# Optimization experiments

Hardware: AMD Instinct MI355X
Metric: run time of the kernel (lower is better)

The kernel has to match this reference:

```python
import jax, jax.numpy as jnp
import numpy as np

B, HW, NL = 32, 1024, 64
VD, LD, H = 1024, 768, 8
EPS = 1e-5


def _bn(x, g, b):
    # x: [B, L, C]; BatchNorm1d (train mode, batch stats) over (B, L) per channel
    m = x.mean(axis=(0, 1), keepdims=True)
    v = x.var(axis=(0, 1), keepdims=True)
    return (x - m) * jax.lax.rsqrt(v + EPS) * g + b


def _inorm(x):
    # x: [B, L, C]; InstanceNorm1d (no affine): normalize over L per (sample, channel)
    m = x.mean(axis=1, keepdims=True)
    v = x.var(axis=1, keepdims=True)
    return (x - m) * jax.lax.rsqrt(v + EPS)


def _sdpa(q_in, k_in, v_in, qw, qb, kw, kb, vw, vb, ow, ob, query_mask=None, key_mask=None):
    b, nq, d = q_in.shape
    nk = k_in.shape[1]
    dk = d // H
    q = (q_in @ qw.T + qb).reshape(b, nq, H, dk).transpose(0, 2, 1, 3)  # [b,h,nq,dk]
    k = (k_in @ kw.T + kb).reshape(b, nk, H, dk).transpose(0, 2, 1, 3)  # [b,h,nk,dk]
    v = (v_in @ vw.T + vb).reshape(b, nk, H, dk).transpose(0, 2, 1, 3)  # [b,h,nk,dk]
    if query_mask is not None:
        q = q * query_mask.reshape(b, 1, nq, 1)
    if key_mask is not None:
        k = k * key_mask.reshape(b, 1, nk, 1)
        v = v * key_mask.reshape(b, 1, nk, 1)
    att = jnp.einsum('bhqd,bhkd->bhqk', q, k) / (dk ** 0.5)
    att = jax.nn.softmax(att, axis=-1)
    out = jnp.einsum('bhqk,bhkd->bhqd', att, v)
    out = out.transpose(0, 2, 1, 3).reshape(b, nq, d)
    return out @ ow.T + ob, att


def setup_inputs() -> dict:
    key = jax.random.key(0)
    ks = iter(jax.random.split(key, 64))
    d = {
        'src': jax.random.normal(next(ks), (B, HW, VD), jnp.float32),
        'lan': jax.random.normal(next(ks), (B, NL, LD), jnp.float32),
        'pos_embed': jax.random.normal(next(ks), (B, HW, VD), jnp.float32),
        'lan_attmask': jnp.ones((B, NL), jnp.float32),
        'ip_w': jax.random.normal(next(ks), (VD, VD), jnp.float32) * 0.02,
        'ip_b': jnp.zeros((VD,), jnp.float32),
        'ip_g': jnp.ones((VD,), jnp.float32),
        'ip_beta': jnp.zeros((VD,), jnp.float32),
        'lp_w': jax.random.normal(next(ks), (VD, LD), jnp.float32) * 0.02,
        'lp_b': jnp.zeros((VD,), jnp.float32),
        'mem_tok': jax.random.normal(next(ks), (1, VD), jnp.float32) * 0.02,
        'neg_mem_tok': jax.random.normal(next(ks), (1, VD), jnp.float32) * 0.02,
    }
    for pre in ('vl', 'mf', 'ff'):
        for nm in ('q', 'k', 'v', 'o'):
            d[f'{pre}_{nm}w'] = jax.random.normal(next(ks), (VD, VD), jnp.float32) * 0.02
            d[f'{pre}_{nm}b'] = jnp.zeros((VD,), jnp.float32)
    d['op_w'] = jax.random.normal(next(ks), (VD, VD), jnp.float32) * 0.02
    d['op_b'] = jnp.zeros((VD,), jnp.float32)
    d['op_g'] = jnp.ones((VD,), jnp.float32)
    d['op_beta'] = jnp.zeros((VD,), jnp.float32)
    return d


def reference(src, lan, pos_embed, lan_attmask, ip_w, ip_b, ip_g, ip_beta, lp_w, lp_b,
              mem_tok, neg_mem_tok,
              vl_qw, vl_qb, vl_kw, vl_kb, vl_vw, vl_vb, vl_ow, vl_ob,
              mf_qw, mf_qb, mf_kw, mf_kb, mf_vw, mf_vb, mf_ow, mf_ob,
              ff_qw, ff_qb, ff_kw, ff_kb, ff_vw, ff_vb, ff_ow, ff_ob,
              op_w, op_b, op_g, op_beta):
    # input/lan projections (Conv1d k=1 == per-token linear), BN on vision path
    src_p = _bn(src @ ip_w.T + ip_b, ip_g, ip_beta)          # [B,HW,VD]
    lan_p = lan @ lp_w.T + lp_b                              # [B,NL,VD]

    # stage 1: vision-language fuse (query = language, multiplicative query mask)
    vl_out, vl_att = _sdpa(lan_p, src_p, src_p,
                           vl_qw, vl_qb, vl_kw, vl_kb, vl_vw, vl_vb, vl_ow, vl_ob,
                           query_mask=lan_attmask)
    # norms[0](vl_out) is computed in the original but its result is never used downstream

    # stage 2: memory fuse (memory tokens attend over language, key mask)
    mem_q = jnp.broadcast_to(mem_tok[None], (B, 1, VD))
    mem_out, mem_att = _sdpa(mem_q, lan_p, lan_p,
                             mf_qw, mf_qb, mf_kw, mf_kb, mf_vw, mf_vb, mf_ow, mf_ob,
                             key_mask=lan_attmask)
    neg_q = jnp.broadcast_to(neg_mem_tok[None], (B, 1, VD))
    cur = jnp.concatenate([neg_q, mem_out], axis=1)          # [B,2,VD]
    cur = _inorm(cur)                                        # norms[1], L=2>1 branch

    # stage 3: feature fuse (vision queries over memory tokens)
    ff_out, ff_att = _sdpa(src_p, cur, cur,
                           ff_qw, ff_qb, ff_kw, ff_kb, ff_vw, ff_vb, ff_ow, ff_ob)
    ff_n = _inorm(ff_out)                                    # norms[2]
    final = _bn(ff_n @ op_w.T + op_b, op_g, op_beta)         # output_proj conv + BN
    return (final, cur, vl_att, mem_att, ff_att)
```

## Files before the change

### kernel.cpp

```cpp
#include <hip/hip_runtime.h>
#include <stdint.h>

#define EPS 1e-5f
#define SCALE 0.08838834764831845f

typedef __bf16 bf16x8 __attribute__((ext_vector_type(8)));
typedef float f32x4 __attribute__((ext_vector_type(4)));
typedef unsigned short u16;
typedef unsigned int u32;
typedef u16 u16x8 __attribute__((ext_vector_type(8)));

__device__ __forceinline__ u16 f2bf(float f) {
  union { float f; u32 u; } x; x.f = f;
  u32 r = x.u + 0x7fffu + ((x.u >> 16) & 1u);
  return (u16)(r >> 16);
}
__device__ __forceinline__ float bf2f(u16 u) {
  union { u32 u; float f; } x; x.u = ((u32)u) << 16; return x.f;
}
__device__ __forceinline__ void glds16(const void* g, void* l) {
  __builtin_amdgcn_global_load_lds((__attribute__((address_space(1))) void*)g,
                                   (__attribute__((address_space(3))) void*)l,
                                   16, 0, 0);
}

struct F2B8 {
  const float* in[8];
  u16* out[8];
  int n4[8];
};
__global__ __launch_bounds__(256) void f2b_multi(F2B8 j) {
  const int seg = blockIdx.y;
  const int n4 = j.n4[seg];
  const float* __restrict__ in = j.in[seg];
  u16* __restrict__ out = j.out[seg];
  for (int i = blockIdx.x * 256 + threadIdx.x; i < n4; i += gridDim.x * 256) {
    float4 v = ((const float4*)in)[i];
    ((ushort4*)out)[i] = make_ushort4(f2bf(v.x), f2bf(v.y), f2bf(v.z), f2bf(v.w));
  }
}

struct WT2 { const float* W[2]; u16* WT[2]; };
__global__ __launch_bounds__(256)
void wtrans2(WT2 g) {
  __shared__ float tile[64][65];
  const float* __restrict__ W = g.W[blockIdx.z];
  u16* __restrict__ WT = g.WT[blockIdx.z];
  const int bx = blockIdx.x, by = blockIdx.y;
  const int r = threadIdx.x >> 2, c0 = (threadIdx.x & 3) * 16;
  const float* src = W + (size_t)(by * 64 + r) * 1024 + bx * 64 + c0;
#pragma unroll
  for (int e = 0; e < 16; e += 4) {
    float4 v = *(const float4*)(src + e);
    tile[r][c0 + e] = v.x; tile[r][c0 + e + 1] = v.y;
    tile[r][c0 + e + 2] = v.z; tile[r][c0 + e + 3] = v.w;
  }
  __syncthreads();
  u16* dst = WT + (size_t)(bx * 64 + r) * 1024 + by * 64 + c0;
#pragma unroll
  for (int e = 0; e < 16; e += 4) {
    ushort4 o = make_ushort4(f2bf(tile[c0 + e][r]), f2bf(tile[c0 + e + 1][r]),
                             f2bf(tile[c0 + e + 2][r]), f2bf(tile[c0 + e + 3][r]));
    *(ushort4*)(dst + e) = o;
  }
}

__global__ __launch_bounds__(256)
void gemm_ip(const float* __restrict__ Af, const u16* __restrict__ B,
             u16* __restrict__ Cb, float* __restrict__ ps,
             float* __restrict__ pq, int M, int N, int K) {
  __shared__ u16 sA[128 * 64];
  __shared__ u16 sB[128 * 64];
  const int nwg = (int)(gridDim.x * gridDim.y);
  const int chunk = nwg >> 3;
  int s = blockIdx.y * gridDim.x + blockIdx.x;
  int t = (s & 7) * chunk + (s >> 3);
  const int bn0 = (t & 7) * 128;
  const int bm0 = (t >> 3) * 128;
  const int tid = threadIdx.x;
  const int w = tid >> 6, l = tid & 63;
  const int wr = w >> 1, wc = w & 1;
  const int lr = l & 15, lk = l >> 4;
  const int swz = lr & 7;

  const int srow = tid >> 3;
  const int lslot = tid & 7;
  const int pslot = lslot ^ (srow & 7);
  const float* As = Af + (size_t)(bm0 + srow) * K + lslot * 8;
  const int scol = pslot << 3;
  const u16* Bb = B + (size_t)(bn0 + srow) * K + scol;
  const size_t rstride32 = (size_t)32 * K;

  f32x4 acc[4][4] = {};
  f32x4 pa0[4], pa1[4];
#pragma unroll
  for (int p = 0; p < 4; ++p) {
    const float* sp = As + (size_t)p * 32 * K;
    pa0[p] = *(const f32x4*)(sp);
    pa1[p] = *(const f32x4*)(sp + 4);
  }

  for (int k0 = 0; k0 < K; k0 += 64) {
#pragma unroll
    for (int p = 0; p < 4; ++p)
      glds16(Bb + p * rstride32 + k0, sB + p * 2048 + w * 512);
#pragma unroll
    for (int p = 0; p < 4; ++p) {
      u16x8 o;
      o[0] = f2bf(pa0[p][0]); o[1] = f2bf(pa0[p][1]);
      o[2] = f2bf(pa0[p][2]); o[3] = f2bf(pa0[p][3]);
      o[4] = f2bf(pa1[p][0]); o[5] = f2bf(pa1[p][1]);
      o[6] = f2bf(pa1[p][2]); o[7] = f2bf(pa1[p][3]);
      *(u16x8*)(sA + p * 2048 + srow * 64 + (pslot << 3)) = o;
    }
    __syncthreads();
    if (k0 + 64 < K) {
#pragma unroll
      for (int p = 0; p < 4; ++p) {
        const float* sp = As + (size_t)p * 32 * K + k0 + 64;
        pa0[p] = *(const f32x4*)(sp);
        pa1[p] = *(const f32x4*)(sp + 4);
      }
    }
#pragma unroll
    for (int ks = 0; ks < 2; ++ks) {
      const int off = (((ks << 2) + lk) ^ swz) << 3;
      bf16x8 af[4], bfr[4];
#pragma unroll
      for (int m = 0; m < 4; ++m)
        af[m] = *(const bf16x8*)(sA + (wr * 64 + m * 16 + lr) * 64 + off);
#pragma unroll
      for (int n = 0; n < 4; ++n)
        bfr[n] = *(const bf16x8*)(sB + (wc * 64 + n * 16 + lr) * 64 + off);
#pragma unroll
      for (int m = 0; m < 4; ++m)
#pragma unroll
        for (int n = 0; n < 4; ++n)
          acc[m][n] = __builtin_amdgcn_mfma_f32_16x16x32_bf16(af[m], bfr[n], acc[m][n], 0, 0, 0);
    }
    __syncthreads();
  }

#pragma unroll
  for (int m = 0; m < 4; ++m) {
    const int grow0 = bm0 + wr * 64 + m * 16 + lk * 4;
#pragma unroll
    for (int n = 0; n < 4; ++n) {
      const int gcol = bn0 + wc * 64 + n * 16 + lr;
#pragma unroll
      for (int i = 0; i < 4; ++i)
        Cb[(size_t)(grow0 + i) * N + gcol] = f2bf(acc[m][n][i]);
    }
  }

  float csum[4], csq[4];
#pragma unroll
  for (int n = 0; n < 4; ++n) {
    float s2 = 0.f, q2 = 0.f;
#pragma unroll
    for (int m = 0; m < 4; ++m)
#pragma unroll
      for (int i = 0; i < 4; ++i) {
        const float v = acc[m][n][i];
        s2 += v; q2 += v * v;
      }
    s2 += __shfl_xor(s2, 16, 64); q2 += __shfl_xor(q2, 16, 64);
    s2 += __shfl_xor(s2, 32, 64); q2 += __shfl_xor(q2, 32, 64);
    csum[n] = s2; csq[n] = q2;
  }
  float* cs = (float*)sA;
  float* cq = cs + 256;
  if (lk == 0) {
#pragma unroll
    for (int n = 0; n < 4; ++n) {
      cs[wr * 128 + wc * 64 + n * 16 + lr] = csum[n];
      cq[wr * 128 + wc * 64 + n * 16 + lr] = csq[n];
    }
  }
  __syncthreads();
  if (tid < 128) {
    const size_t o = (size_t)(bm0 >> 7) * 1024 + bn0 + tid;
    ps[o] = cs[tid] + cs[128 + tid];
    pq[o] = cq[tid] + cq[128 + tid];
  }
}

__global__ __launch_bounds__(256)
void gemm_bt(const u16* __restrict__ A, const u16* __restrict__ B,
             const float* __restrict__ bias, u16* __restrict__ Cb,
             int M, int N, int K) {
  __shared__ u16 sA[128 * 64];
  __shared__ u16 sB[128 * 64];
  const int nwg = (int)(gridDim.x * gridDim.y);
  const int chunk = nwg >> 3;
  int s = blockIdx.y * gridDim.x + blockIdx.x;
  int t = (s & 7) * chunk + (s >> 3);
  const int bn0 = (t & 7) * 128;
  const int bm0 = (t >> 3) * 128;
  const int tid = threadIdx.x;
  const int w = tid >> 6, l = tid & 63;
  const int wr = w >> 1, wc = w & 1;
  const int lr = l & 15, lk = l >> 4;
  const int swz = lr & 7;

  const int srow = tid >> 3;
  const int scol = ((tid & 7) ^ (srow & 7)) << 3;
  const u16* Ab = A + (size_t)(bm0 + srow) * K + scol;
  const u16* Bb = B + (size_t)(bn0 + srow) * K + scol;
  const size_t rstride32 = (size_t)32 * K;

  f32x4 acc[4][4] = {};

  for (int k0 = 0; k0 < K; k0 += 64) {
#pragma unroll
    for (int p = 0; p < 4; ++p) {
      glds16(Ab + p * rstride32 + k0, sA + p * 2048 + w * 512);
      glds16(Bb + p * rstride32 + k0, sB + p * 2048 + w * 512);
    }
    __syncthreads();
#pragma unroll
    for (int ks = 0; ks < 2; ++ks) {
      const int off = (((ks << 2) + lk) ^ swz) << 3;
      bf16x8 af[4], bfr[4];
#pragma unroll
      for (int m = 0; m < 4; ++m)
        af[m] = *(const bf16x8*)(sA + (wr * 64 + m * 16 + lr) * 64 + off);
#pragma unroll
      for (int n = 0; n < 4; ++n)
        bfr[n] = *(const bf16x8*)(sB + (wc * 64 + n * 16 + lr) * 64 + off);
#pragma unroll
      for (int m = 0; m < 4; ++m)
#pragma unroll
        for (int n = 0; n < 4; ++n)
          acc[m][n] = __builtin_amdgcn_mfma_f32_16x16x32_bf16(af[m], bfr[n], acc[m][n], 0, 0, 0);
    }
    __syncthreads();
  }

#pragma unroll
  for (int m = 0; m < 4; ++m) {
    const int grow0 = bm0 + wr * 64 + m * 16 + lk * 4;
#pragma unroll
    for (int n = 0; n < 4; ++n) {
      const int gcol = bn0 + wc * 64 + n * 16 + lr;
      const float bv = bias ? bias[gcol] : 0.0f;
#pragma unroll
      for (int i = 0; i < 4; ++i) {
        const float v = acc[m][n][i] + bv;
        Cb[(size_t)(grow0 + i) * N + gcol] = f2bf(v);
      }
    }
  }
}

struct G3 { const u16* B[3]; const float* bias[3]; u16* C[3]; };
__global__ __launch_bounds__(256)
void gemm_bt_z(const u16* __restrict__ A, G3 g, int M, int N, int K) {
  __shared__ u16 sA[128 * 64];
  __shared__ u16 sB[128 * 64];
  const int z = blockIdx.z;
  const u16* __restrict__ B = g.B[z];
  const float* __restrict__ bias = g.bias[z];
  u16* __restrict__ Cb = g.C[z];
  const int nwg = (int)(gridDim.x * gridDim.y);
  const int chunk = nwg >> 3;
  int s = blockIdx.y * gridDim.x + blockIdx.x;
  int t = (s & 7) * chunk + (s >> 3);
  const int bn0 = (t & 7) * 128;
  const int bm0 = (t >> 3) * 128;
  const int tid = threadIdx.x;
  const int w = tid >> 6, l = tid & 63;
  const int wr = w >> 1, wc = w & 1;
  const int lr = l & 15, lk = l >> 4;
  const int swz = lr & 7;

  const int srow = tid >> 3;
  const int scol = ((tid & 7) ^ (srow & 7)) << 3;
  const u16* Ab = A + (size_t)(bm0 + srow) * K + scol;
  const u16* Bb = B + (size_t)(bn0 + srow) * K + scol;
  const size_t rstride32 = (size_t)32 * K;

  f32x4 acc[4][4] = {};

  for (int k0 = 0; k0 < K; k0 += 64) {
#pragma unroll
    for (int p = 0; p < 4; ++p) {
      glds16(Ab + p * rstride32 + k0, sA + p * 2048 + w * 512);
      glds16(Bb + p * rstride32 + k0, sB + p * 2048 + w * 512);
    }
    __syncthreads();
#pragma unroll
    for (int ks = 0; ks < 2; ++ks) {
      const int off = (((ks << 2) + lk) ^ swz) << 3;
      bf16x8 af[4], bfr[4];
#pragma unroll
      for (int m = 0; m < 4; ++m)
        af[m] = *(const bf16x8*)(sA + (wr * 64 + m * 16 + lr) * 64 + off);
#pragma unroll
      for (int n = 0; n < 4; ++n)
        bfr[n] = *(const bf16x8*)(sB + (wc * 64 + n * 16 + lr) * 64 + off);
#pragma unroll
      for (int m = 0; m < 4; ++m)
#pragma unroll
        for (int n = 0; n < 4; ++n)
          acc[m][n] = __builtin_amdgcn_mfma_f32_16x16x32_bf16(af[m], bfr[n], acc[m][n], 0, 0, 0);
    }
    __syncthreads();
  }

#pragma unroll
  for (int m = 0; m < 4; ++m) {
    const int grow0 = bm0 + wr * 64 + m * 16 + lk * 4;
#pragma unroll
    for (int n = 0; n < 4; ++n) {
      const int gcol = bn0 + wc * 64 + n * 16 + lr;
      const float bv = bias[gcol];
#pragma unroll
      for (int i = 0; i < 4; ++i)
        Cb[(size_t)(grow0 + i) * N + gcol] = f2bf(acc[m][n][i] + bv);
    }
  }
}

__global__ __launch_bounds__(256)
void gemm_qpp(const u16* __restrict__ QV, const u16* __restrict__ WT,
              const float* __restrict__ afv, u16* __restrict__ Q2) {
  __shared__ u16 sA[128 * 64];
  __shared__ u16 sB[128 * 64];
  const int h = blockIdx.z;
  int s = blockIdx.y * 8 + blockIdx.x;
  int t = (s & 7) * 16 + (s >> 3);
  const int bn0 = (t & 7) * 128;
  const int bm0 = (t >> 3) * 128;
  const int tid = threadIdx.x;
  const int w = tid >> 6, l = tid & 63;
  const int wr = w >> 1, wc = w & 1;
  const int lr = l & 15, lk = l >> 4;
  const int swz = lr & 7;

  const int srow = tid >> 3;
  const int scol = ((tid & 7) ^ (srow & 7)) << 3;
  const u16* Ab = QV + (size_t)(bm0 + srow) * 1024 + h * 128 + scol;
  const u16* Bb = WT + (size_t)(bn0 + srow) * 1024 + h * 128 + scol;
  const size_t rstride32 = (size_t)32 * 1024;

  f32x4 acc[4][4] = {};

  for (int k0 = 0; k0 < 128; k0 += 64) {
#pragma unroll
    for (int p = 0; p < 4; ++p) {
      glds16(Ab + p * rstride32 + k0, sA + p * 2048 + w * 512);
      glds16(Bb + p * rstride32 + k0, sB + p * 2048 + w * 512);
    }
    __syncthreads();
#pragma unroll
    for (int ks = 0; ks < 2; ++ks) {
      const int off = (((ks << 2) + lk) ^ swz) << 3;
      bf16x8 af[4], bfr[4];
#pragma unroll
      for (int m = 0; m < 4; ++m)
        af[m] = *(const bf16x8*)(sA + (wr * 64 + m * 16 + lr) * 64 + off);
#pragma unroll
      for (int n = 0; n < 4; ++n)
        bfr[n] = *(const bf16x8*)(sB + (wc * 64 + n * 16 + lr) * 64 + off);
#pragma unroll
      for (int m = 0; m < 4; ++m)
#pragma unroll
        for (int n = 0; n < 4; ++n)
          acc[m][n] = __builtin_amdgcn_mfma_f32_16x16x32_bf16(af[m], bfr[n], acc[m][n], 0, 0, 0);
    }
    __syncthreads();
  }

#pragma unroll
  for (int m = 0; m < 4; ++m) {
    const int grow0 = bm0 + wr * 64 + m * 16 + lk * 4;
#pragma unroll
    for (int n = 0; n < 4; ++n) {
      const int gcol = bn0 + wc * 64 + n * 16 + lr;
      const float a = afv[gcol];
#pragma unroll
      for (int i = 0; i < 4; ++i) {
        const int gr = grow0 + i;
        const int q2row = ((gr >> 6) << 9) + h * 64 + (gr & 63);
        Q2[(size_t)q2row * 1024 + gcol] = f2bf(acc[m][n][i] * a);
      }
    }
  }
}

__global__ __launch_bounds__(256)
void cst_kernel(const u16* __restrict__ QV, const float* __restrict__ wcv,
                float* __restrict__ cstv) {
  const int row = blockIdx.x * 256 + threadIdx.x;
  const int b = row >> 9, rem = row & 511;
  const int h = rem >> 6, i = rem & 63;
  const u16* q = QV + (size_t)(b * 64 + i) * 1024 + h * 128;
  const float* wv = wcv + h * 128;
  float acc = 0.f;
  for (int d = 0; d < 128; d += 8) {
    u16x8 v = *(const u16x8*)(q + d);
#pragma unroll
    for (int e = 0; e < 8; ++e) acc += bf2f(v[e]) * wv[d + e];
  }
  cstv[row] = acc;
}

__global__ __launch_bounds__(512)
void vl_fused(const u16* __restrict__ Q2, const u16* __restrict__ Y1,
              const float* __restrict__ cstv, const float* __restrict__ qmask,
              float* __restrict__ out) {
  __shared__ u16 sB[1024 * 32];
  __shared__ u16 sA[32 * 32];
  __shared__ float redmx[32][8];
  __shared__ float redsm[32][8];
  const int blk = blockIdx.x;
  const int xcd = blk & 7;
  const int idx = blk >> 3;
  const int b = xcd + 8 * (idx >> 4);
  const int r0 = (idx & 15) * 32;
  const int tid = threadIdx.x;
  const int w = tid >> 6, l = tid & 63;
  const int lr = l & 15, lk = l >> 4;

  const int arow = tid >> 2;
  const int aslot = tid & 3;
  const u16* Asrc = Q2 + (size_t)(b * 512 + r0 + arow) * 1024 +
                    ((aslot ^ (arow & 3)) << 3);
  const int brow0 = w * 16 + (l >> 2);
  const int bslot = l & 3;
  const u16* Bsrc0 = Y1 + (size_t)b * 1048576 + (size_t)brow0 * 1024 +
                     ((bslot ^ ((l >> 2) & 3)) << 3);

  f32x4 acc[2][8] = {};

  for (int k0 = 0; k0 < 1024; k0 += 32) {
    if (tid < 128) glds16(Asrc + k0, sA + w * 512);
#pragma unroll
    for (int p = 0; p < 8; ++p)
      glds16(Bsrc0 + (size_t)p * 128 * 1024 + k0, sB + (p * 8 + w) * 512);
    __syncthreads();
    const int roff = (lk ^ (lr & 3)) << 3;
    bf16x8 af[2];
#pragma unroll
    for (int m = 0; m < 2; ++m)
      af[m] = *(const bf16x8*)(sA + (m * 16 + lr) * 32 + roff);
#pragma unroll
    for (int n = 0; n < 8; ++n) {
      bf16x8 bf_ = *(const bf16x8*)(sB + (w * 128 + n * 16 + lr) * 32 + roff);
      acc[0][n] = __builtin_amdgcn_mfma_f32_16x16x32_bf16(af[0], bf_, acc[0][n], 0, 0, 0);
      acc[1][n] = __builtin_amdgcn_mfma_f32_16x16x32_bf16(af[1], bf_, acc[1][n], 0, 0, 0);
    }
    __syncthreads();
  }

  float cst_r[2][4], scl[2][4];
#pragma unroll
  for (int m = 0; m < 2; ++m)
#pragma unroll
    for (int i = 0; i < 4; ++i) {
      const int rem = r0 + m * 16 + lk * 4 + i;
      cst_r[m][i] = cstv[b * 512 + rem];
      scl[m][i] = qmask[b * 64 + (rem & 63)] * SCALE;
    }
#pragma unroll
  for (int m = 0; m < 2; ++m)
#pragma unroll
    for (int n = 0; n < 8; ++n)
#pragma unroll
      for (int i = 0; i < 4; ++i)
        acc[m][n][i] = (acc[m][n][i] + cst_r[m][i]) * scl[m][i];

  float mx[2][4];
#pragma unroll
  for (int m = 0; m < 2; ++m)
#pragma unroll
    for (int i = 0; i < 4; ++i) {
      float v = -3.4e38f;
#pragma unroll
      for (int n = 0; n < 8; ++n) v = fmaxf(v, acc[m][n][i]);
      for (int o = 1; o < 16; o <<= 1) v = fmaxf(v, __shfl_xor(v, o, 64));
      mx[m][i] = v;
    }
  if (lr == 0) {
#pragma unroll
    for (int m = 0; m < 2; ++m)
#pragma unroll
      for (int i = 0; i < 4; ++i)
        redmx[m * 16 + lk * 4 + i][w] = mx[m][i];
  }
  __syncthreads();
#pragma unroll
  for (int m = 0; m < 2; ++m)
#pragma unroll
    for (int i = 0; i < 4; ++i) {
      const int rl = m * 16 + lk * 4 + i;
      float v = redmx[rl][0];
#pragma unroll
      for (int ww = 1; ww < 8; ++ww) v = fmaxf(v, redmx[rl][ww]);
      mx[m][i] = v;
    }

  float sm[2][4];
#pragma unroll
  for (int m = 0; m < 2; ++m)
#pragma unroll
    for (int i = 0; i < 4; ++i) {
      float s = 0.f;
#pragma unroll
      for (int n = 0; n < 8; ++n) {
        float e = expf(acc[m][n][i] - mx[m][i]);
        acc[m][n][i] = e;
        s += e;
      }
      for (int o = 1; o < 16; o <<= 1) s += __shfl_xor(s, o, 64);
      sm[m][i] = s;
    }
  if (lr == 0) {
#pragma unroll
    for (int m = 0; m < 2; ++m)
#pragma unroll
      for (int i = 0; i < 4; ++i)
        redsm[m * 16 + lk * 4 + i][w] = sm[m][i];
  }
  __syncthreads();
#pragma unroll
  for (int m = 0; m < 2; ++m)
#pragma unroll
    for (int i = 0; i < 4; ++i) {
      const int rl = m * 16 + lk * 4 + i;
      float s = 0.f;
#pragma unroll
      for (int ww = 0; ww < 8; ++ww) s += redsm[rl][ww];
      sm[m][i] = 1.0f / s;
    }

#pragma unroll
  for (int m = 0; m < 2; ++m)
#pragma unroll
    for (int i = 0; i < 4; ++i) {
      const size_t grow = (size_t)(b * 512 + r0 + m * 16 + lk * 4 + i);
#pragma unroll
      for (int n = 0; n < 8; ++n)
        out[grow * 1024 + w * 128 + n * 16 + lr] = acc[m][n][i] * sm[m][i];
    }
}

__global__ __launch_bounds__(256)
void colstats_final(const float* __restrict__ ps, const float* __restrict__ pq,
                    float2* __restrict__ st, const float* __restrict__ g,
                    const float* __restrict__ be, float* __restrict__ afv,
                    float* __restrict__ cfv, float inv_n) {
  __shared__ float rs_[8][32], rq_[8][32];
  const int cg = threadIdx.x >> 5, cl = threadIdx.x & 31;
  const int col = blockIdx.x * 32 + cl;
  float s = 0.f, q = 0.f;
  for (int i = 0; i < 32; ++i) {
    const size_t idx = (size_t)(cg * 32 + i) * 1024 + col;
    s += ps[idx]; q += pq[idx];
  }
  rs_[cg][cl] = s; rq_[cg][cl] = q;
  __syncthreads();
  if (cg == 0) {
    for (int i = 1; i < 8; ++i) { s += rs_[i][cl]; q += rq_[i][cl]; }
    const float m = s * inv_n;
    const float v = q * inv_n - m * m;
    const float rs = rsqrtf(v + EPS);
    st[col] = make_float2(m, rs);
    if (afv) {
      const float a = rs * g[col];
      afv[col] = a;
      cfv[col] = be[col] - m * a;
    }
  }
}

__global__ __launch_bounds__(256)
void small_gemm(const float* __restrict__ A, const float* __restrict__ W,
                const float* __restrict__ bias, float* __restrict__ out,
                int N, int K) {
  __shared__ float sA[1024];
  const int m = blockIdx.y;
  const int n = blockIdx.x * 256 + threadIdx.x;
  for (int i = threadIdx.x; i < K; i += 256) sA[i] = A[(size_t)m * K + i];
  __syncthreads();
  const float4* w4 = (const float4*)(W + (size_t)n * K);
  const float4* a4 = (const float4*)sA;
  float acc = bias ? bias[n] : 0.0f;
  for (int k = 0; k < K / 4; ++k) {
    float4 wv = w4[k], av = a4[k];
    acc += av.x * wv.x + av.y * wv.y + av.z * wv.z + av.w * wv.w;
  }
  out[(size_t)m * N + n] = acc;
}

struct SG2 { const float* W[2]; const float* bias[2]; float* out[2]; };
__global__ __launch_bounds__(256)
void small_gemm2(const float* __restrict__ A, SG2 g, int N, int K) {
  __shared__ float sA[1024];
  const int z = blockIdx.z;
  const int m = blockIdx.y;
  const int n = blockIdx.x * 256 + threadIdx.x;
  for (int i = threadIdx.x; i < K; i += 256) sA[i] = A[(size_t)m * K + i];
  __syncthreads();
  const float4* w4 = (const float4*)(g.W[z] + (size_t)n * K);
  const float4* a4 = (const float4*)sA;
  float acc = g.bias[z][n];
  for (int k = 0; k < K / 4; ++k) {
    float4 wv = w4[k], av = a4[k];
    acc += av.x * wv.x + av.y * wv.y + av.z * wv.z + av.w * wv.w;
  }
  g.out[z][(size_t)m * N + n] = acc;
}

__global__ __launch_bounds__(256)
void mem_attn(const float* __restrict__ qmf, const u16* __restrict__ KM,
              const u16* __restrict__ VM, const float* __restrict__ mask,
              float* __restrict__ att_out, float* __restrict__ attv_out) {
  __shared__ float qs[1024];
  __shared__ float sS[512];
  __shared__ float sP[512];
  __shared__ float sM[64];
  const int b = blockIdx.x;
  const int tid = threadIdx.x;
  for (int i = tid; i < 1024; i += 256) qs[i] = qmf[i];
  if (tid < 64) sM[tid] = mask[b * 64 + tid];
  __syncthreads();
  for (int p = tid; p < 512; p += 256) {
    const int h = p >> 6, j = p & 63;
    const u16* kr = KM + (size_t)(b * 64 + j) * 1024 + h * 128;
    float acc = 0.f;
    for (int d = 0; d < 128; ++d) acc += qs[h * 128 + d] * bf2f(kr[d]);
    sS[p] = acc * sM[j] * SCALE;
  }
  __syncthreads();
  if (tid < 8) {
    const int h = tid;
    float mx = -3.4e38f;
    for (int j = 0; j < 64; ++j) mx = fmaxf(mx, sS[h * 64 + j]);
    float sum = 0.f;
    for (int j = 0; j < 64; ++j) {
      float e = expf(sS[h * 64 + j] - mx);
      sP[h * 64 + j] = e; sum += e;
    }
    const float inv = 1.0f / sum;
    for (int j = 0; j < 64; ++j) {
      float pp = sP[h * 64 + j] * inv;
      sP[h * 64 + j] = pp;
      att_out[(size_t)(b * 8 + h) * 64 + j] = pp;
    }
  }
  __syncthreads();
  for (int c = tid; c < 1024; c += 256) {
    const int h = c >> 7;
    float acc = 0.f;
    for (int j = 0; j < 64; ++j)
      acc += sP[h * 64 + j] * sM[j] * bf2f(VM[(size_t)(b * 64 + j) * 1024 + c]);
    attv_out[(size_t)b * 1024 + c] = acc;
  }
}

__global__ __launch_bounds__(256)
void make_cur(const float* __restrict__ neg, const float* __restrict__ memo,
              float* __restrict__ cur_out, float* __restrict__ curw) {
  const int i = blockIdx.x * 256 + threadIdx.x;
  const int b = i >> 10, c = i & 1023;
  const float a = neg[c], x = memo[i];
  const float mean = 0.5f * (a + x);
  const float d = a - mean;
  const float rs = rsqrtf(d * d + EPS);
  const float o0 = d * rs, o1 = -d * rs;
  cur_out[(size_t)(b * 2) * 1024 + c] = o0;
  cur_out[(size_t)(b * 2 + 1) * 1024 + c] = o1;
  curw[(size_t)(b * 2) * 1024 + c] = o0;
  curw[(size_t)(b * 2 + 1) * 1024 + c] = o1;
}

__global__ __launch_bounds__(256)
void ffw_fold(const float* __restrict__ kff, const float* __restrict__ wfq,
              const float* __restrict__ qb, const float* __restrict__ afv,
              const float* __restrict__ cfv, u16* __restrict__ w2ff,
              float* __restrict__ cff) {
  __shared__ float redl[4];
  const int b = blockIdx.y, jh = blockIdx.x;
  const int j = jh >> 3, h = jh & 7;
  const int tid = threadIdx.x;
  const int m0 = tid * 4;
  const float* kp = kff + (size_t)b * 2048 + j * 1024 + h * 128;
  float a0 = 0, a1 = 0, a2 = 0, a3 = 0;
  for (int n = 0; n < 128; ++n) {
    const float kv = kp[n];
    const float4 wv = *(const float4*)(wfq + (size_t)(h * 128 + n) * 1024 + m0);
    a0 += kv * wv.x; a1 += kv * wv.y; a2 += kv * wv.z; a3 += kv * wv.w;
  }
  float cpart = a0 * cfv[m0] + a1 * cfv[m0 + 1] + a2 * cfv[m0 + 2] + a3 * cfv[m0 + 3];
  if (tid < 128) cpart += qb[h * 128 + tid] * kp[tid];
  ushort4 o = make_ushort4(f2bf(a0 * afv[m0]), f2bf(a1 * afv[m0 + 1]),
                           f2bf(a2 * afv[m0 + 2]), f2bf(a3 * afv[m0 + 3]));
  *(ushort4*)(w2ff + (size_t)(b * 16 + jh) * 1024 + m0) = o;
  for (int o2 = 32; o2 > 0; o2 >>= 1) cpart += __shfl_xor(cpart, o2, 64);
  if ((tid & 63) == 0) redl[tid >> 6] = cpart;
  __syncthreads();
  if (tid == 0) cff[b * 16 + jh] = redl[0] + redl[1] + redl[2] + redl[3];
}

__global__ __launch_bounds__(256)
void ff_score(const u16* __restrict__ Y1, const u16* __restrict__ w2ff,
              const float* __restrict__ cff, float* __restrict__ P,
              float* __restrict__ att_out) {
  __shared__ u16 sA[128 * 64];
  __shared__ u16 sB[16 * 1024];
  const int chunk = blockIdx.x, b = blockIdx.y;
  const int tid = threadIdx.x;
  const int w = tid >> 6, l = tid & 63;
  const int lr = l & 15, lk = l >> 4;
  const int swz = lr & 7;

  {
    const int n = tid >> 4;
    const int sb = (tid & 15) * 8;
#pragma unroll
    for (int v = 0; v < 8; ++v) {
      const int sidx = sb + v;
      u16x8 val = *(const u16x8*)(w2ff + (size_t)(b * 16 + n) * 1024 + sidx * 8);
      *(u16x8*)(sB + n * 1024 + ((sidx ^ (n & 7)) << 3)) = val;
    }
  }

  const int srow = tid >> 3;
  const int scol = ((tid & 7) ^ (srow & 7)) << 3;
  const u16* Ab = Y1 + ((size_t)(b * 1024 + chunk * 128) + srow) * 1024 + scol;
  const size_t rstride32 = (size_t)32 * 1024;

  f32x4 acc[2] = {};

  for (int k0 = 0; k0 < 1024; k0 += 64) {
#pragma unroll
    for (int p = 0; p < 4; ++p)
      glds16(Ab + p * rstride32 + k0, sA + p * 2048 + w * 512);
    __syncthreads();
#pragma unroll
    for (int ks = 0; ks < 2; ++ks) {
      const int off = (((ks << 2) + lk) ^ swz) << 3;
      bf16x8 a0 = *(const bf16x8*)(sA + (w * 32 + lr) * 64 + off);
      bf16x8 a1 = *(const bf16x8*)(sA + (w * 32 + 16 + lr) * 64 + off);
      const int bs = (k0 >> 3) + (ks << 2) + lk;
      bf16x8 bf_ = *(const bf16x8*)(sB + lr * 1024 + ((bs ^ swz) << 3));
      acc[0] = __builtin_amdgcn_mfma_f32_16x16x32_bf16(a0, bf_, acc[0], 0, 0, 0);
      acc[1] = __builtin_amdgcn_mfma_f32_16x16x32_bf16(a1, bf_, acc[1], 0, 0, 0);
    }
    __syncthreads();
  }

  const float cadd = cff[b * 16 + lr];
  const int h = lr & 7, jj = lr >> 3;
#pragma unroll
  for (int m = 0; m < 2; ++m)
#pragma unroll
    for (int i = 0; i < 4; ++i) {
      const float sval = (acc[m][i] + cadd) * SCALE;
      const float other = __shfl_xor(sval, 8, 64);
      const float mx = fmaxf(sval, other);
      const float e0 = expf(sval - mx), e1 = expf(other - mx);
      const float p = e0 / (e0 + e1);
      const int trow = chunk * 128 + w * 32 + m * 16 + lk * 4 + i;
      P[((size_t)b * 1024 + trow) * 16 + lr] = p;
      att_out[((size_t)(b * 8 + h) * 1024 + trow) * 2 + jj] = p;
    }
}

__global__ __launch_bounds__(256)
void pg_kernel(const float* __restrict__ P, float* __restrict__ G,
               float* __restrict__ pbar) {
  __shared__ float Pl[128][16];
  const int b = blockIdx.x;
  const int tid = threadIdx.x;
  const int j = tid >> 4, j2 = tid & 15;
  float acc = 0.f, accp = 0.f;
  for (int c = 0; c < 8; ++c) {
    __syncthreads();
    for (int i = tid; i < 2048; i += 256)
      Pl[i >> 4][i & 15] = P[((size_t)b * 1024 + c * 128 + (i >> 4)) * 16 + (i & 15)];
    __syncthreads();
    for (int t = 0; t < 128; ++t) {
      acc += Pl[t][j] * Pl[t][j2];
      if (j == 0) accp += Pl[t][j2];
    }
  }
  G[b * 256 + tid] = acc * (1.f / 1024.f);
  if (j == 0) pbar[b * 16 + j2] = accp * (1.f / 1024.f);
}

__global__ __launch_bounds__(256)
void ufold(const float* __restrict__ vff, const u16* __restrict__ wfoT,
           float* __restrict__ U) {
  const int b = blockIdx.y, jh = blockIdx.x;
  const int j = jh >> 3, h = jh & 7;
  const int m0 = threadIdx.x * 4;
  const float* vp = vff + (size_t)b * 2048 + j * 1024 + h * 128;
  float a0 = 0, a1 = 0, a2 = 0, a3 = 0;
  for (int d = 0; d < 128; ++d) {
    const float kv = vp[d];
    ushort4 wv = *(const ushort4*)(wfoT + (size_t)(h * 128 + d) * 1024 + m0);
    a0 += kv * bf2f(wv.x); a1 += kv * bf2f(wv.y);
    a2 += kv * bf2f(wv.z); a3 += kv * bf2f(wv.w);
  }
  *(float4*)(U + (size_t)(b * 16 + jh) * 1024 + m0) = make_float4(a0, a1, a2, a3);
}

__global__ __launch_bounds__(256)
void iprep(const float* __restrict__ U, const float* __restrict__ G,
           const float* __restrict__ pbar, const float* __restrict__ ob,
           u16* __restrict__ U2b) {
  __shared__ float Gs[256], pb[16];
  const int b = blockIdx.x;
  const int tid = threadIdx.x;
  Gs[tid] = G[b * 256 + tid];
  if (tid < 16) pb[tid] = pbar[b * 16 + tid];
  __syncthreads();
  const int m0 = tid * 4;
  float rr[4], mi4[4];
#pragma unroll
  for (int e = 0; e < 4; ++e) {
    const int m = m0 + e;
    float u[16];
#pragma unroll
    for (int jj = 0; jj < 16; ++jj) u[jj] = U[(size_t)(b * 16 + jj) * 1024 + m];
    const float o = ob[m];
    float s1 = 0.f;
#pragma unroll
    for (int jj = 0; jj < 16; ++jj) s1 += pb[jj] * u[jj];
    float q = 0.f;
#pragma unroll
    for (int jj = 0; jj < 16; ++jj) {
      float gq = 0.f;
#pragma unroll
      for (int j2 = 0; j2 < 16; ++j2) gq += Gs[jj * 16 + j2] * u[j2];
      q += u[jj] * gq;
    }
    const float mean = s1 + o;
    const float e2 = q + 2.f * o * s1 + o * o;
    const float var = fmaxf(e2 - mean * mean, 0.f);
    mi4[e] = mean;
    rr[e] = rsqrtf(var + EPS);
  }
#pragma unroll
  for (int jj = 0; jj < 16; ++jj) {
    float4 u4 = *(const float4*)(U + (size_t)(b * 16 + jj) * 1024 + m0);
    ushort4 o = make_ushort4(f2bf(u4.x * rr[0]), f2bf(u4.y * rr[1]),
                             f2bf(u4.z * rr[2]), f2bf(u4.w * rr[3]));
    *(ushort4*)(U2b + (size_t)(b * 32 + jj) * 1024 + m0) = o;
  }
  float4 ob4 = *(const float4*)(ob + m0);
  ushort4 od = make_ushort4(
      f2bf((ob4.x - mi4[0]) * rr[0]), f2bf((ob4.y - mi4[1]) * rr[1]),
      f2bf((ob4.z - mi4[2]) * rr[2]), f2bf((ob4.w - mi4[3]) * rr[3]));
  *(ushort4*)(U2b + (size_t)(b * 32 + 16) * 1024 + m0) = od;
  ushort4 z = make_ushort4(0, 0, 0, 0);
#pragma unroll
  for (int jj = 17; jj < 32; ++jj)
    *(ushort4*)(U2b + (size_t)(b * 32 + jj) * 1024 + m0) = z;
}

__global__ __launch_bounds__(256)
void w2op_gemm(const u16* __restrict__ U2b, const u16* __restrict__ wop,
               float* __restrict__ W2op) {
  __shared__ u16 sA[32 * 64];
  __shared__ u16 sB[128 * 64];
  const int b = blockIdx.y;
  const int bn0 = blockIdx.x * 128;
  const int tid = threadIdx.x;
  const int w = tid >> 6, l = tid & 63;
  const int lr = l & 15, lk = l >> 4;
  const int swz = lr & 7;
  const int srow = tid >> 3;
  const int scol = ((tid & 7) ^ (srow & 7)) << 3;
  const u16* Ab = U2b + (size_t)b * 32768 + (size_t)srow * 1024 + scol;
  const u16* Bb = wop + (size_t)(bn0 + srow) * 1024 + scol;
  const size_t rstride32 = (size_t)32 * 1024;

  f32x4 acc[2][2] = {};
  for (int k0 = 0; k0 < 1024; k0 += 64) {
    glds16(Ab + k0, sA + w * 512);
#pragma unroll
    for (int p = 0; p < 4; ++p)
      glds16(Bb + p * rstride32 + k0, sB + p * 2048 + w * 512);
    __syncthreads();
#pragma unroll
    for (int ks = 0; ks < 2; ++ks) {
      const int off = (((ks << 2) + lk) ^ swz) << 3;
      bf16x8 af[2], bfr[2];
#pragma unroll
      for (int m = 0; m < 2; ++m)
        af[m] = *(const bf16x8*)(sA + (m * 16 + lr) * 64 + off);
#pragma unroll
      for (int n = 0; n < 2; ++n)
        bfr[n] = *(const bf16x8*)(sB + (w * 32 + n * 16 + lr) * 64 + off);
#pragma unroll
      for (int m = 0; m < 2; ++m)
#pragma unroll
        for (int n = 0; n < 2; ++n)
          acc[m][n] = __builtin_amdgcn_mfma_f32_16x16x32_bf16(af[m], bfr[n], acc[m][n], 0, 0, 0);
    }
    __syncthreads();
  }
#pragma unroll
  for (int m = 0; m < 2; ++m)
#pragma unroll
    for (int n = 0; n < 2; ++n)
#pragma unroll
      for (int i = 0; i < 4; ++i) {
        const int row = m * 16 + lk * 4 + i;
        const int col = bn0 + w * 32 + n * 16 + lr;
        W2op[((size_t)b * 32 + row) * 1024 + col] = acc[m][n][i];
      }
}

__global__ __launch_bounds__(256)
void znstats_part(const float* __restrict__ W2op, const float* __restrict__ G,
                  const float* __restrict__ pbar, float* __restrict__ pmu,
                  float* __restrict__ pe2) {
  __shared__ float Gs[256], pb[16];
  const int m = blockIdx.x * 256 + threadIdx.x;
  const int bg = blockIdx.y;
  float amu = 0.f, ae2 = 0.f;
  for (int bi = 0; bi < 4; ++bi) {
    const int b = bg * 4 + bi;
    __syncthreads();
    Gs[threadIdx.x] = G[b * 256 + threadIdx.x];
    if (threadIdx.x < 16) pb[threadIdx.x] = pbar[b * 16 + threadIdx.x];
    __syncthreads();
    float wv[17];
#pragma unroll
    for (int jj = 0; jj < 17; ++jj) wv[jj] = W2op[((size_t)b * 32 + jj) * 1024 + m];
    float s1 = 0.f;
#pragma unroll
    for (int jj = 0; jj < 16; ++jj) s1 += pb[jj] * wv[jj];
    float q = 0.f;
#pragma unroll
    for (int jj = 0; jj < 16; ++jj) {
      float gq = 0.f;
#pragma unroll
      for (int j2 = 0; j2 < 16; ++j2) gq += Gs[jj * 16 + j2] * wv[j2];
      q += wv[jj] * gq;
    }
    const float cz = wv[16];
    amu += s1 + cz;
    ae2 += q + 2.f * cz * s1 + cz * cz;
  }
  pmu[bg * 1024 + m] = amu;
  pe2[bg * 1024 + m] = ae2;
}

__global__ __launch_bounds__(256)
void znfin(const float* __restrict__ pmu, const float* __restrict__ pe2,
           const float* __restrict__ g, const float* __restrict__ be,
           float* __restrict__ afin, float* __restrict__ cf0) {
  const int m = blockIdx.x * 256 + threadIdx.x;
  float mu = 0.f, e2 = 0.f;
#pragma unroll
  for (int i = 0; i < 8; ++i) { mu += pmu[i * 1024 + m]; e2 += pe2[i * 1024 + m]; }
  mu *= (1.f / 32.f); e2 *= (1.f / 32.f);
  const float var = fmaxf(e2 - mu * mu, 0.f);
  const float A = rsqrtf(var + EPS) * g[m];
  afin[m] = A;
  cf0[m] = be[m] - mu * A;
}

__global__ __launch_bounds__(256)
void zfinal(const float* __restrict__ P, const float* __restrict__ W2op,
            const float* __restrict__ afin, const float* __restrict__ cf0,
            float* __restrict__ out) {
  __shared__ float PL[512];
  const int blk = blockIdx.x;
  const int b = blk >> 5;
  const int r0 = blk * 32;
  const int tid = threadIdx.x;
  const int col = tid * 4;

  f32x4 A4 = *(const f32x4*)(afin + col);
  f32x4 wreg[17];
#pragma unroll
  for (int jj = 0; jj < 17; ++jj) {
    f32x4 wv = *(const f32x4*)(W2op + ((size_t)b * 32 + jj) * 1024 + col);
    wreg[jj] = wv * A4;
  }
  const f32x4 basev = wreg[16] + *(const f32x4*)(cf0 + col);

  if (tid < 128)
    ((f32x4*)PL)[tid] = *(const f32x4*)(P + (size_t)r0 * 16 + tid * 4);
  __syncthreads();

  float* obase = out + (size_t)r0 * 1024 + col;
  for (int r = 0; r < 32; ++r) {
    const float* pr = PL + r * 16;
    f32x4 a = basev;
#pragma unroll
    for (int jj = 0; jj < 16; ++jj) a += pr[jj] * wreg[jj];
    *(f32x4*)(obase + (size_t)r * 1024) = a;
  }
}

extern "C" void kernel_launch(void* const* d_in, const int* in_sizes, int n_in,
                              void* d_out, int out_size, void* d_ws, size_t ws_size,
                              hipStream_t stream) {
  (void)in_sizes; (void)n_in; (void)out_size; (void)ws_size;

  const float* src      = (const float*)d_in[0];
  const float* lan      = (const float*)d_in[1];
  const float* qmask    = (const float*)d_in[3];
  const float* ip_w     = (const float*)d_in[4];
  const float* ip_g     = (const float*)d_in[6];
  const float* ip_beta  = (const float*)d_in[7];
  const float* lp_w     = (const float*)d_in[8];
  const float* lp_b     = (const float*)d_in[9];
  const float* mem_tok  = (const float*)d_in[10];
  const float* neg_tok  = (const float*)d_in[11];
  const float* vl_qw    = (const float*)d_in[12];
  const float* vl_qb    = (const float*)d_in[13];
  const float* vl_kw    = (const float*)d_in[14];
  const float* vl_kb    = (const float*)d_in[15];
  const float* mf_qw    = (const float*)d_in[20];
  const float* mf_qb    = (const float*)d_in[21];
  const float* mf_kw    = (const float*)d_in[22];
  const float* mf_kb    = (const float*)d_in[23];
  const float* mf_vw    = (const float*)d_in[24];
  const float* mf_vb    = (const float*)d_in[25];
  const float* mf_ow    = (const float*)d_in[26];
  const float* mf_ob    = (const float*)d_in[27];
  const float* ff_qw    = (const float*)d_in[28];
  const float* ff_qb    = (const float*)d_in[29];
  const float* ff_kw    = (const float*)d_in[30];
  const float* ff_kb    = (const float*)d_in[31];
  const float* ff_vw    = (const float*)d_in[32];
  const float* ff_vb    = (const float*)d_in[33];
  const float* ff_ow    = (const float*)d_in[34];
  const float* ff_ob    = (const float*)d_in[35];
  const float* op_w     = (const float*)d_in[36];
  const float* op_g     = (const float*)d_in[38];
  const float* op_beta  = (const float*)d_in[39];

  float* out_final = (float*)d_out;
  float* out_cur   = out_final + 33554432ull;
  float* out_vl    = out_cur + 65536ull;
  float* out_mem   = out_vl + 16777216ull;
  float* out_ff    = out_mem + 16384ull;

  char* wp = (char*)d_ws;
  auto take = [&](size_t sz) { char* r = wp; wp += (sz + 255) & ~(size_t)255; return r; };
  u16*   W1   = (u16*)  take(67108864);
  u16*   W2   = (u16*)  take(67108864);
  u16*   LP   = (u16*)  take(4194304);
  u16*   QV   = (u16*)  take(4194304);
  u16*   KM   = (u16*)  take(4194304);
  u16*   VM   = (u16*)  take(4194304);
  u16*   LANB = (u16*)  take(3145728);
  u16*   wip  = (u16*)  take(2097152);
  u16*   wlp  = (u16*)  take(1572864);
  u16*   wvq  = (u16*)  take(2097152);
  u16*   wmk  = (u16*)  take(2097152);
  u16*   wmv  = (u16*)  take(2097152);
  u16*   wop  = (u16*)  take(2097152);
  u16*   wvkT = (u16*)  take(2097152);
  u16*   wfoT = (u16*)  take(2097152);
  u16*   w2ff = (u16*)  take(1048576);
  u16*   U2b  = (u16*)  take(2097152);
  float* qmf   = (float*)take(4096);
  float* attvm = (float*)take(131072);
  float* memo  = (float*)take(131072);
  float* curw  = (float*)take(262144);
  float* kff   = (float*)take(262144);
  float* vff   = (float*)take(262144);
  float* ps    = (float*)take(1048576);
  float* pq    = (float*)take(1048576);
  float2* st1  = (float2*)take(8192);
  float* afv   = (float*)take(4096);
  float* cfv   = (float*)take(4096);
  float* wcv   = (float*)take(4096);
  float* cff   = (float*)take(2048);
  float* Pbuf  = (float*)take(2097152);
  float* Ub    = (float*)take(2097152);
  float* W2opb = (float*)take(4194304);
  float* Gb    = (float*)take(32768);
  float* pbarb = (float*)take(2048);
  float* pmu   = (float*)take(32768);
  float* pe2   = (float*)take(32768);
  float* afin  = (float*)take(4096);
  float* cf0   = (float*)take(4096);
  float* cstv  = (float*)take(65536);

  const dim3 blk(256);

  {
    F2B8 j;
    const float* ins[7] = {lan, ip_w, lp_w, vl_qw, mf_kw, mf_vw, op_w};
    u16* outs[7] = {LANB, wip, wlp, wvq, wmk, wmv, wop};
    int n4s[7] = {393216, 262144, 196608, 262144, 262144, 262144, 262144};
    for (int i = 0; i < 7; ++i) { j.in[i] = ins[i]; j.out[i] = outs[i]; j.n4[i] = n4s[i]; }
    f2b_multi<<<dim3(1024, 7), blk, 0, stream>>>(j);
  }
  {
    WT2 g;
    g.W[0] = vl_kw; g.WT[0] = wvkT;
    g.W[1] = ff_ow; g.WT[1] = wfoT;
    wtrans2<<<dim3(16, 16, 2), blk, 0, stream>>>(g);
  }

  gemm_ip<<<dim3(8, 256), blk, 0, stream>>>(src, wip, W2, ps, pq, 32768, 1024, 1024);
  colstats_final<<<dim3(32), blk, 0, stream>>>(ps, pq, st1, ip_g, ip_beta, afv, cfv, 1.0f / 32768.0f);

  gemm_bt<<<dim3(8, 16), blk, 0, stream>>>(LANB, wlp, lp_b, LP, 2048, 1024, 768);
  {
    G3 g;
    g.B[0] = wvq; g.bias[0] = vl_qb; g.C[0] = QV;
    g.B[1] = wmk; g.bias[1] = mf_kb; g.C[1] = KM;
    g.B[2] = wmv; g.bias[2] = mf_vb; g.C[2] = VM;
    gemm_bt_z<<<dim3(8, 16, 3), blk, 0, stream>>>(LP, g, 2048, 1024, 1024);
  }

  gemm_qpp<<<dim3(8, 16, 8), blk, 0, stream>>>(QV, wvkT, afv, W1);
  small_gemm<<<dim3(4, 1), blk, 0, stream>>>(cfv, vl_kw, vl_kb, wcv, 1024, 1024);
  cst_kernel<<<dim3(64), blk, 0, stream>>>(QV, wcv, cstv);
  vl_fused<<<dim3(512), dim3(512), 0, stream>>>(W1, W2, cstv, qmask, out_vl);

  small_gemm<<<dim3(4, 1), blk, 0, stream>>>(mem_tok, mf_qw, mf_qb, qmf, 1024, 1024);
  mem_attn<<<dim3(32), blk, 0, stream>>>(qmf, KM, VM, qmask, out_mem, attvm);
  small_gemm<<<dim3(4, 32), blk, 0, stream>>>(attvm, mf_ow, mf_ob, memo, 1024, 1024);
  make_cur<<<dim3(128), blk, 0, stream>>>(neg_tok, memo, out_cur, curw);

  {
    SG2 g;
    g.W[0] = ff_kw; g.bias[0] = ff_kb; g.out[0] = kff;
    g.W[1] = ff_vw; g.bias[1] = ff_vb; g.out[1] = vff;
    small_gemm2<<<dim3(4, 64, 2), blk, 0, stream>>>(curw, g, 1024, 1024);
  }
  ffw_fold<<<dim3(16, 32), blk, 0, stream>>>(kff, ff_qw, ff_qb, afv, cfv, w2ff, cff);
  ff_score<<<dim3(8, 32), blk, 0, stream>>>(W2, w2ff, cff, Pbuf, out_ff);
  pg_kernel<<<dim3(32), blk, 0, stream>>>(Pbuf, Gb, pbarb);
  ufold<<<dim3(16, 32), blk, 0, stream>>>(vff, wfoT, Ub);
  iprep<<<dim3(32), blk, 0, stream>>>(Ub, Gb, pbarb, ff_ob, U2b);
  w2op_gemm<<<dim3(8, 32), blk, 0, stream>>>(U2b, wop, W2opb);
  znstats_part<<<dim3(4, 8), blk, 0, stream>>>(W2opb, Gb, pbarb, pmu, pe2);
  znfin<<<dim3(4), blk, 0, stream>>>(pmu, pe2, op_g, op_beta, afin, cf0);
  zfinal<<<dim3(1024), blk, 0, stream>>>(Pbuf, W2opb, afin, cf0, out_final);
}
```

Baseline: 676.1 us.

## Enlarge M-tiles in input-projection GEMM and fused vision-language attention kernel

```diff
diff --git a/kernel.cpp b/kernel.cpp
--- a/kernel.cpp
+++ b/kernel.cpp
@@ -65,62 +65,57 @@
   }
 }
 
-__global__ __launch_bounds__(256)
+__global__ __launch_bounds__(512)
 void gemm_ip(const float* __restrict__ Af, const u16* __restrict__ B,
              u16* __restrict__ Cb, float* __restrict__ ps,
              float* __restrict__ pq, int M, int N, int K) {
-  __shared__ u16 sA[128 * 64];
+  __shared__ u16 sA[256 * 64];
   __shared__ u16 sB[128 * 64];
   const int nwg = (int)(gridDim.x * gridDim.y);
   const int chunk = nwg >> 3;
   int s = blockIdx.y * gridDim.x + blockIdx.x;
   int t = (s & 7) * chunk + (s >> 3);
   const int bn0 = (t & 7) * 128;
-  const int bm0 = (t >> 3) * 128;
+  const int bm0 = (t >> 3) * 256;
   const int tid = threadIdx.x;
   const int w = tid >> 6, l = tid & 63;
-  const int wr = w >> 1, wc = w & 1;
+  const int wm = w >> 1, wn = w & 1;
   const int lr = l & 15, lk = l >> 4;
   const int swz = lr & 7;
 
-  const int srow = tid >> 3;
-  const int lslot = tid & 7;
-  const int pslot = lslot ^ (srow & 7);
-  const float* As = Af + (size_t)(bm0 + srow) * K + lslot * 8;
-  const int scol = pslot << 3;
-  const u16* Bb = B + (size_t)(bn0 + srow) * K + scol;
-  const size_t rstride32 = (size_t)32 * K;
+  const int ar = tid & 255;
+  const int qh = tid >> 8;
+  const float* As = Af + (size_t)(bm0 + ar) * K + qh * 32;
+  const int srow_b = tid >> 3;
+  const int scol_b = ((tid & 7) ^ (srow_b & 7)) << 3;
+  const u16* Bb = B + (size_t)(bn0 + srow_b) * K + scol_b;
+  const size_t rstride64 = (size_t)64 * K;
 
   f32x4 acc[4][4] = {};
-  f32x4 pa0[4], pa1[4];
-#pragma unroll
-  for (int p = 0; p < 4; ++p) {
-    const float* sp = As + (size_t)p * 32 * K;
-    pa0[p] = *(const f32x4*)(sp);
-    pa1[p] = *(const f32x4*)(sp + 4);
-  }
+  f32x4 pa[8];
+#pragma unroll
+  for (int p = 0; p < 8; ++p) pa[p] = *(const f32x4*)(As + p * 4);
 
   for (int k0 = 0; k0 < K; k0 += 64) {
 #pragma unroll
-    for (int p = 0; p < 4; ++p)
-      glds16(Bb + p * rstride32 + k0, sB + p * 2048 + w * 512);
-#pragma unroll
-    for (int p = 0; p < 4; ++p) {
+    for (int p = 0; p < 2; ++p)
+      glds16(Bb + p * rstride64 + k0, sB + p * 4096 + w * 512);
+#pragma unroll
+    for (int jj = 0; jj < 4; ++jj) {
+      const int sl = qh * 4 + jj;
+      const int pslot = sl ^ (ar & 7);
       u16x8 o;
-      o[0] = f2bf(pa0[p][0]); o[1] = f2bf(pa0[p][1]);
-      o[2] = f2bf(pa0[p][2]); o[3] = f2bf(pa0[p][3]);
-      o[4] = f2bf(pa1[p][0]); o[5] = f2bf(pa1[p][1]);
-      o[6] = f2bf(pa1[p][2]); o[7] = f2bf(pa1[p][3]);
-      *(u16x8*)(sA + p * 2048 + srow * 64 + (pslot << 3)) = o;
+      o[0] = f2bf(pa[2 * jj][0]); o[1] = f2bf(pa[2 * jj][1]);
+      o[2] = f2bf(pa[2 * jj][2]); o[3] = f2bf(pa[2 * jj][3]);
+      o[4] = f2bf(pa[2 * jj + 1][0]); o[5] = f2bf(pa[2 * jj + 1][1]);
+      o[6] = f2bf(pa[2 * jj + 1][2]); o[7] = f2bf(pa[2 * jj + 1][3]);
+      *(u16x8*)(sA + ar * 64 + (pslot << 3)) = o;
     }
     __syncthreads();
     if (k0 + 64 < K) {
 #pragma unroll
-      for (int p = 0; p < 4; ++p) {
-        const float* sp = As + (size_t)p * 32 * K + k0 + 64;
-        pa0[p] = *(const f32x4*)(sp);
-        pa1[p] = *(const f32x4*)(sp + 4);
-      }
+      for (int p = 0; p < 8; ++p)
+        pa[p] = *(const f32x4*)(As + k0 + 64 + p * 4);
     }
 #pragma unroll
     for (int ks = 0; ks < 2; ++ks) {
@@ -128,10 +123,10 @@
       bf16x8 af[4], bfr[4];
 #pragma unroll
       for (int m = 0; m < 4; ++m)
-        af[m] = *(const bf16x8*)(sA + (wr * 64 + m * 16 + lr) * 64 + off);
+        af[m] = *(const bf16x8*)(sA + (wm * 64 + m * 16 + lr) * 64 + off);
 #pragma unroll
       for (int n = 0; n < 4; ++n)
-        bfr[n] = *(const bf16x8*)(sB + (wc * 64 + n * 16 + lr) * 64 + off);
+        bfr[n] = *(const bf16x8*)(sB + (wn * 64 + n * 16 + lr) * 64 + off);
 #pragma unroll
       for (int m = 0; m < 4; ++m)
 #pragma unroll
@@ -143,10 +138,10 @@
 
 #pragma unroll
   for (int m = 0; m < 4; ++m) {
-    const int grow0 = bm0 + wr * 64 + m * 16 + lk * 4;
+    const int grow0 = bm0 + wm * 64 + m * 16 + lk * 4;
 #pragma unroll
     for (int n = 0; n < 4; ++n) {
-      const int gcol = bn0 + wc * 64 + n * 16 + lr;
+      const int gcol = bn0 + wn * 64 + n * 16 + lr;
 #pragma unroll
       for (int i = 0; i < 4; ++i)
         Cb[(size_t)(grow0 + i) * N + gcol] = f2bf(acc[m][n][i]);
@@ -169,19 +164,19 @@
     csum[n] = s2; csq[n] = q2;
   }
   float* cs = (float*)sA;
-  float* cq = cs + 256;
+  float* cq = cs + 512;
   if (lk == 0) {
 #pragma unroll
     for (int n = 0; n < 4; ++n) {
-      cs[wr * 128 + wc * 64 + n * 16 + lr] = csum[n];
-      cq[wr * 128 + wc * 64 + n * 16 + lr] = csq[n];
+      cs[wm * 128 + wn * 64 + n * 16 + lr] = csum[n];
+      cq[wm * 128 + wn * 64 + n * 16 + lr] = csq[n];
     }
   }
   __syncthreads();
   if (tid < 128) {
-    const size_t o = (size_t)(bm0 >> 7) * 1024 + bn0 + tid;
-    ps[o] = cs[tid] + cs[128 + tid];
-    pq[o] = cq[tid] + cq[128 + tid];
+    const size_t o = (size_t)(bm0 >> 8) * 1024 + bn0 + tid;
+    ps[o] = cs[tid] + cs[128 + tid] + cs[256 + tid] + cs[384 + tid];
+    pq[o] = cq[tid] + cq[128 + tid] + cq[256 + tid] + cq[384 + tid];
   }
 }
 
@@ -411,14 +406,14 @@
               const float* __restrict__ cstv, const float* __restrict__ qmask,
               float* __restrict__ out) {
   __shared__ u16 sB[1024 * 32];
-  __shared__ u16 sA[32 * 32];
-  __shared__ float redmx[32][8];
-  __shared__ float redsm[32][8];
+  __shared__ u16 sA[64 * 32];
+  __shared__ float redmx[64][8];
+  __shared__ float redsm[64][8];
   const int blk = blockIdx.x;
   const int xcd = blk & 7;
   const int idx = blk >> 3;
-  const int b = xcd + 8 * (idx >> 4);
-  const int r0 = (idx & 15) * 32;
+  const int b = xcd + 8 * (idx >> 3);
+  const int r0 = (idx & 7) * 64;
   const int tid = threadIdx.x;
   const int w = tid >> 6, l = tid & 63;
   const int lr = l & 15, lk = l >> 4;
@@ -432,31 +427,32 @@
   const u16* Bsrc0 = Y1 + (size_t)b * 1048576 + (size_t)brow0 * 1024 +
                      ((bslot ^ ((l >> 2) & 3)) << 3);
 
-  f32x4 acc[2][8] = {};
+  f32x4 acc[4][8] = {};
 
   for (int k0 = 0; k0 < 1024; k0 += 32) {
-    if (tid < 128) glds16(Asrc + k0, sA + w * 512);
+    if (tid < 256) glds16(Asrc + k0, sA + w * 512);
 #pragma unroll
     for (int p = 0; p < 8; ++p)
       glds16(Bsrc0 + (size_t)p * 128 * 1024 + k0, sB + (p * 8 + w) * 512);
     __syncthreads();
     const int roff = (lk ^ (lr & 3)) << 3;
-    bf16x8 af[2];
-#pragma unroll
-    for (int m = 0; m < 2; ++m)
+    bf16x8 af[4];
+#pragma unroll
+    for (int m = 0; m < 4; ++m)
       af[m] = *(const bf16x8*)(sA + (m * 16 + lr) * 32 + roff);
 #pragma unroll
     for (int n = 0; n < 8; ++n) {
       bf16x8 bf_ = *(const bf16x8*)(sB + (w * 128 + n * 16 + lr) * 32 + roff);
-      acc[0][n] = __builtin_amdgcn_mfma_f32_16x16x32_bf16(af[0], bf_, acc[0][n], 0, 0, 0);
-      acc[1][n] = __builtin_amdgcn_mfma_f32_16x16x32_bf16(af[1], bf_, acc[1][n], 0, 0, 0);
-    }
-    __syncthreads();
-  }
-
-  float cst_r[2][4], scl[2][4];
-#pragma unroll
-  for (int m = 0; m < 2; ++m)
+#pragma unroll
+      for (int m = 0; m < 4; ++m)
+        acc[m][n] = __builtin_amdgcn_mfma_f32_16x16x32_bf16(af[m], bf_, acc[m][n], 0, 0, 0);
+    }
+    __syncthreads();
+  }
+
+  float cst_r[4][4], scl[4][4];
+#pragma unroll
+  for (int m = 0; m < 4; ++m)
 #pragma unroll
     for (int i = 0; i < 4; ++i) {
       const int rem = r0 + m * 16 + lk * 4 + i;
@@ -464,16 +460,16 @@
       scl[m][i] = qmask[b * 64 + (rem & 63)] * SCALE;
     }
 #pragma unroll
-  for (int m = 0; m < 2; ++m)
+  for (int m = 0; m < 4; ++m)
 #pragma unroll
     for (int n = 0; n < 8; ++n)
 #pragma unroll
       for (int i = 0; i < 4; ++i)
         acc[m][n][i] = (acc[m][n][i] + cst_r[m][i]) * scl[m][i];
 
-  float mx[2][4];
-#pragma unroll
-  for (int m = 0; m < 2; ++m)
+  float mx[4][4];
+#pragma unroll
+  for (int m = 0; m < 4; ++m)
 #pragma unroll
     for (int i = 0; i < 4; ++i) {
       float v = -3.4e38f;
@@ -484,14 +480,14 @@
     }
   if (lr == 0) {
 #pragma unroll
-    for (int m = 0; m < 2; ++m)
+    for (int m = 0; m < 4; ++m)
 #pragma unroll
       for (int i = 0; i < 4; ++i)
         redmx[m * 16 + lk * 4 + i][w] = mx[m][i];
   }
   __syncthreads();
 #pragma unroll
-  for (int m = 0; m < 2; ++m)
+  for (int m = 0; m < 4; ++m)
 #pragma unroll
     for (int i = 0; i < 4; ++i) {
       const int rl = m * 16 + lk * 4 + i;
@@ -501,9 +497,9 @@
       mx[m][i] = v;
     }
 
-  float sm[2][4];
-#pragma unroll
-  for (int m = 0; m < 2; ++m)
+  float sm[4][4];
+#pragma unroll
+  for (int m = 0; m < 4; ++m)
 #pragma unroll
     for (int i = 0; i < 4; ++i) {
       float s = 0.f;
@@ -518,14 +514,14 @@
     }
   if (lr == 0) {
 #pragma unroll
-    for (int m = 0; m < 2; ++m)
+    for (int m = 0; m < 4; ++m)
 #pragma unroll
       for (int i = 0; i < 4; ++i)
         redsm[m * 16 + lk * 4 + i][w] = sm[m][i];
   }
   __syncthreads();
 #pragma unroll
-  for (int m = 0; m < 2; ++m)
+  for (int m = 0; m < 4; ++m)
 #pragma unroll
     for (int i = 0; i < 4; ++i) {
       const int rl = m * 16 + lk * 4 + i;
@@ -536,7 +532,7 @@
     }
 
 #pragma unroll
-  for (int m = 0; m < 2; ++m)
+  for (int m = 0; m < 4; ++m)
 #pragma unroll
     for (int i = 0; i < 4; ++i) {
       const size_t grow = (size_t)(b * 512 + r0 + m * 16 + lk * 4 + i);
@@ -555,8 +551,8 @@
   const int cg = threadIdx.x >> 5, cl = threadIdx.x & 31;
   const int col = blockIdx.x * 32 + cl;
   float s = 0.f, q = 0.f;
-  for (int i = 0; i < 32; ++i) {
-    const size_t idx = (size_t)(cg * 32 + i) * 1024 + col;
+  for (int i = 0; i < 16; ++i) {
+    const size_t idx = (size_t)(cg * 16 + i) * 1024 + col;
     s += ps[idx]; q += pq[idx];
   }
   rs_[cg][cl] = s; rq_[cg][cl] = q;
@@ -1106,7 +1102,7 @@
     wtrans2<<<dim3(16, 16, 2), blk, 0, stream>>>(g);
   }
 
-  gemm_ip<<<dim3(8, 256), blk, 0, stream>>>(src, wip, W2, ps, pq, 32768, 1024, 1024);
+  gemm_ip<<<dim3(8, 128), dim3(512), 0, stream>>>(src, wip, W2, ps, pq, 32768, 1024, 1024);
   colstats_final<<<dim3(32), blk, 0, stream>>>(ps, pq, st1, ip_g, ip_beta, afv, cfv, 1.0f / 32768.0f);
 
   gemm_bt<<<dim3(8, 16), blk, 0, stream>>>(LANB, wlp, lp_b, LP, 2048, 1024, 768);
@@ -1121,7 +1117,7 @@
   gemm_qpp<<<dim3(8, 16, 8), blk, 0, stream>>>(QV, wvkT, afv, W1);
   small_gemm<<<dim3(4, 1), blk, 0, stream>>>(cfv, vl_kw, vl_kb, wcv, 1024, 1024);
   cst_kernel<<<dim3(64), blk, 0, stream>>>(QV, wcv, cstv);
-  vl_fused<<<dim3(512), dim3(512), 0, stream>>>(W1, W2, cstv, qmask, out_vl);
+  vl_fused<<<dim3(256), dim3(512), 0, stream>>>(W1, W2, cstv, qmask, out_vl);
 
   small_gemm<<<dim3(4, 1), blk, 0, stream>>>(mem_tok, mf_qw, mf_qb, qmf, 1024, 1024);
   mem_attn<<<dim3(32), blk, 0, stream>>>(qmf, KM, VM, qmask, out_mem, attvm);
```

Result: slower. 747.9 us (+10.6%).
